# Kernel optimization log

Hardware: AMD Instinct MI355X
Metric: run time of the kernel (lower is better)

Reference implementation:

```python
import jax, jax.numpy as jnp
import numpy as np

EPS = 1e-5


def farthest_point_sample(points, npoint):
    # points: [B, N, 3]; returns idx [B, npoint] (int32)
    B, N, _ = points.shape
    # is_center=True: start from the point farthest from the centroid
    centroid = points.mean(axis=1, keepdims=True)            # [B,1,3]
    d0 = jnp.sum((points - centroid) ** 2, axis=-1)           # [B,N]
    farthest = jnp.argmax(d0, axis=-1)                        # [B]
    distance = jnp.full((B, N), 1e10, dtype=points.dtype)

    def step(carry, _):
        dist, far = carry
        cent = jnp.take_along_axis(points, far[:, None, None], axis=1)  # [B,1,3]
        d = jnp.sum((points - cent) ** 2, axis=-1)                       # [B,N]
        dist = jnp.minimum(dist, d)
        new_far = jnp.argmax(dist, axis=-1)
        return (dist, new_far), far

    (_, _), idx = jax.lax.scan(step, (distance, farthest), None, length=npoint)
    return idx.T  # [B, npoint]


def index_points(x, idx):
    # x: [B, N, C], idx: [B, S] -> [B, S, C]
    return jnp.take_along_axis(x, idx[:, :, None], axis=1)


def setup_inputs() -> dict:
    key = jax.random.key(0)
    k1, k2, k3, k4 = jax.random.split(key, 4)
    B, N, in_dim, out_dim = 8, 16384, 128, 256
    points = jax.random.normal(k1, (B, N, 3), dtype=jnp.float32)
    features = jax.random.normal(k2, (B, N, in_dim), dtype=jnp.float32)
    W = jax.random.normal(k3, (out_dim, in_dim), dtype=jnp.float32) * (1.0 / np.sqrt(in_dim))
    b = jax.random.normal(k4, (out_dim,), dtype=jnp.float32) * 0.01
    return {"points": points, "features": features, "W": W, "b": b, "num_points": 4096}


def reference(points, features, W, b, num_points):
    # conv1x1 on features.transpose(-1,-2): [B,in,N] -> [B,out,N]
    x = jnp.einsum('bnc,oc->bon', features, W) + b[None, :, None]  # [B,out,N]
    # InstanceNorm1d (affine=False): normalize over spatial dim N per (b, channel)
    mu = x.mean(axis=-1, keepdims=True)
    var = x.var(axis=-1, keepdims=True)
    x = (x - mu) * jax.lax.rsqrt(var + EPS)
    x = jax.nn.relu(x)
    feats = x.transpose(0, 2, 1)  # [B,N,out]

    idx = farthest_point_sample(points, num_points)  # [B, num_points]
    sampled_points = index_points(points, idx)
    sampled_features = index_points(feats, idx)
    return sampled_points, sampled_features
```

## Files before the change

kernel.cpp:

```cpp
#include <hip/hip_runtime.h>
#include <math.h>

#define B_      8
#define N_      16384
#define CIN_    128
#define COUT_   256
#define NS_     4096
#define FPS_T   1024
#define PPT     16

#define RPT16(X) X(0) X(1) X(2) X(3) X(4) X(5) X(6) X(7) \
                 X(8) X(9) X(10) X(11) X(12) X(13) X(14) X(15)

static __device__ __forceinline__ float sqdist_xla(float px, float py, float pz,
                                                   float cx, float cy, float cz) {
  float dx = __fsub_rn(px, cx);
  float dy = __fsub_rn(py, cy);
  float dz = __fsub_rn(pz, cz);
  return __fmaf_rn(dz, dz, __fmaf_rn(dy, dy, __fmul_rn(dx, dx)));
}

__global__ __launch_bounds__(1024, 4) void k1_fps_gram(
    const float* __restrict__ points, const float* __restrict__ features,
    float* __restrict__ outP, int* __restrict__ idxw,
    float* __restrict__ Gpart, float* __restrict__ Spart)
{
  const int tid = threadIdx.x;
  if (blockIdx.x < B_) {
    const int b = blockIdx.x;
    const float* __restrict__ P = points + (size_t)b * N_ * 3;
    const int base = tid * PPT;
    const int lane = tid & 63;
    const int wid  = tid >> 6;

    #define DECLP(i) float px##i, py##i, pz##i, dd##i;
    RPT16(DECLP)
    #define LOADP(i) px##i = P[3*(base+(i))+0]; \
                     py##i = P[3*(base+(i))+1]; \
                     pz##i = P[3*(base+(i))+2];
    RPT16(LOADP)

    __shared__ unsigned svv[16];
    __shared__ int      sii[16];
    __shared__ float    cC[3];
    __shared__ float    cent[3];

    if (tid < 3) {
      const int c = tid;
      float acc = P[c];
      for (int n = 1; n < N_; ++n) acc = __fadd_rn(acc, P[3*n + c]);
      cent[c] = __fmul_rn(acc, 6.103515625e-05f);
    }
    __syncthreads();
    const float cx0 = cent[0], cy0 = cent[1], cz0 = cent[2];

    auto select_far = [&](float lmv, int lkv, int s) {
      unsigned long long pk =
          ((unsigned long long)__float_as_uint(lmv) << 32) | (unsigned)(~(base + lkv));
      #pragma unroll
      for (int off = 32; off > 0; off >>= 1) {
        unsigned long long op = __shfl_xor(pk, off);
        pk = (op > pk) ? op : pk;
      }
      if (lane == 0) { svv[wid] = (unsigned)(pk >> 32); sii[wid] = (int)(~(unsigned)pk); }
      __syncthreads();
      if (wid == 0) {
        unsigned long long p2 = 0ULL;
        if (lane < 16)
          p2 = ((unsigned long long)svv[lane] << 32) | (unsigned)(~sii[lane]);
        #pragma unroll
        for (int off = 8; off > 0; off >>= 1) {
          unsigned long long op = __shfl_xor(p2, off);
          p2 = (op > p2) ? op : p2;
        }
        if (lane == 0) {
          const int bi = (int)(~(unsigned)p2);
          const float* cp = P + 3 * (size_t)bi;
          const float x = cp[0], y = cp[1], z = cp[2];
          cC[0] = x; cC[1] = y; cC[2] = z;
          const size_t ob = (size_t)b * NS_ + s;
          outP[ob*3+0] = x; outP[ob*3+1] = y; outP[ob*3+2] = z;
          idxw[b*NS_ + s] = bi;
        }
      }
      __syncthreads();
    };

    {
      float lm = -1.0f; int lk = 0;
      #define SCAN0(i) { float d = sqdist_xla(px##i, py##i, pz##i, cx0, cy0, cz0); \
                         dd##i = d; bool bt = (d > lm); \
                         lk = bt ? (i) : lk; lm = bt ? d : lm; }
      RPT16(SCAN0)
      select_far(lm, lk, 0);
    }
    #define INITD(i) dd##i = 1e10f;
    RPT16(INITD)

    for (int s = 1; s < NS_; ++s) {
      const float ccx = cC[0], ccy = cC[1], ccz = cC[2];
      float lm = -1.0f; int lk = 0;
      #define SCANU(i) { float d = sqdist_xla(px##i, py##i, pz##i, ccx, ccy, ccz); \
                         float nd = fminf(dd##i, d); dd##i = nd; \
                         bool bt = (nd > lm); \
                         lk = bt ? (i) : lk; lm = bt ? nd : lm; }
      RPT16(SCANU)
      select_far(lm, lk, s);
    }
  } else {
    const int gb = (int)blockIdx.x - B_;
    const int b  = gb >> 3;
    const int ch = gb & 7;
    __shared__ float Lf[32][128];
    float acc[4][4];
    #pragma unroll
    for (int i = 0; i < 4; ++i)
      #pragma unroll
      for (int j = 0; j < 4; ++j) acc[i][j] = 0.f;
    float sacc = 0.f;
    const int ti = tid >> 5;
    const int tj = tid & 31;
    const float* fb = features + ((size_t)b * N_ + (size_t)ch * 2048) * CIN_;
    for (int t32 = 0; t32 < 64; ++t32) {
      const float4 v0 = *(const float4*)(fb + ((size_t)t32 * 32 + ti) * CIN_ + tj * 4);
      __syncthreads();
      *(float4*)&Lf[ti][tj*4] = v0;
      __syncthreads();
      #pragma unroll 4
      for (int r = 0; r < 32; ++r) {
        const float4 a4 = *(const float4*)&Lf[r][ti*4];
        const float4 b4 = *(const float4*)&Lf[r][tj*4];
        const float av[4] = {a4.x, a4.y, a4.z, a4.w};
        const float bw[4] = {b4.x, b4.y, b4.z, b4.w};
        #pragma unroll
        for (int i = 0; i < 4; ++i)
          #pragma unroll
          for (int j = 0; j < 4; ++j) acc[i][j] = fmaf(av[i], bw[j], acc[i][j]);
      }
      if (tid < 128) {
        #pragma unroll 8
        for (int r = 0; r < 32; ++r) sacc += Lf[r][tid];
      }
    }
    float* gp = Gpart + (size_t)gb * (CIN_*CIN_);
    #pragma unroll
    for (int i = 0; i < 4; ++i)
      #pragma unroll
      for (int j = 0; j < 4; ++j)
        gp[(ti*4+i)*CIN_ + tj*4 + j] = acc[i][j];
    if (tid < 128) Spart[gb*CIN_ + tid] = sacc;
  }
}

__global__ void k2a_reduce(const float* __restrict__ Gpart, const float* __restrict__ Spart,
                           float* __restrict__ Gred, float* __restrict__ Sred)
{
  const int b = blockIdx.x;
  for (int i = threadIdx.x; i < CIN_*CIN_; i += blockDim.x) {
    float s = 0.f;
    #pragma unroll
    for (int c = 0; c < 8; ++c) s += Gpart[((size_t)(b*8+c))*(CIN_*CIN_) + i];
    Gred[(size_t)b*(CIN_*CIN_) + i] = s;
  }
  if (threadIdx.x < CIN_) {
    float s = 0.f;
    #pragma unroll
    for (int c = 0; c < 8; ++c) s += Spart[(b*8+c)*CIN_ + threadIdx.x];
    Sred[b*CIN_ + threadIdx.x] = s;
  }
}

__global__ __launch_bounds__(128) void k2b_stats(
    const float* __restrict__ Gred, const float* __restrict__ Sred,
    const float* __restrict__ W, const float* __restrict__ bias,
    float* __restrict__ stats)
{
  const int b = blockIdx.x >> 8;
  const int o = blockIdx.x & 255;
  const int tid = threadIdx.x;
  __shared__ float sw[CIN_];
  __shared__ float r1[CIN_], r2[CIN_];
  sw[tid] = W[(size_t)o*CIN_ + tid];
  __syncthreads();
  const float* gr = Gred + (size_t)b*CIN_*CIN_ + (size_t)tid*CIN_;
  float g = 0.f;
  #pragma unroll 8
  for (int j = 0; j < CIN_; ++j) g = fmaf(gr[j], sw[j], g);
  r1[tid] = g * sw[tid];
  r2[tid] = sw[tid] * Sred[b*CIN_ + tid];
  __syncthreads();
  for (int stp = 64; stp > 0; stp >>= 1) {
    if (tid < stp) { r1[tid] += r1[tid+stp]; r2[tid] += r2[tid+stp]; }
    __syncthreads();
  }
  if (tid == 0) {
    const float wGw = r1[0], wS = r2[0], bo = bias[o];
    const float invN = 1.0f / (float)N_;
    const float mu  = wS*invN + bo;
    const float ex2 = (wGw + 2.0f*bo*wS)*invN + bo*bo;
    float var = ex2 - mu*mu;
    var = fmaxf(var, 0.0f);
    const float sc = 1.0f / sqrtf(var + 1e-5f);
    stats[((size_t)(b*COUT_ + o))*2 + 0] = wS*invN;
    stats[((size_t)(b*COUT_ + o))*2 + 1] = sc;
  }
}

__global__ __launch_bounds__(256) void k3_out(
    const float* __restrict__ features, const float* __restrict__ W,
    const int* __restrict__ idxw, const float* __restrict__ stats,
    float* __restrict__ outF)
{
  const int tid = threadIdx.x;
  const int b  = blockIdx.x >> 8;
  const int r  = blockIdx.x & 255;
  const int st = r >> 2, ot = r & 3;
  const int s0 = st * 64, o0 = ot * 64;

  __shared__ float Fs[64][129];
  __shared__ float Wt[64][129];
  __shared__ int   sIdx[64];
  __shared__ float sSub[64], sSc[64];

  if (tid < 64) sIdx[tid] = idxw[b*NS_ + s0 + tid];
  if (tid >= 64 && tid < 128) {
    const int oo = tid - 64;
    sSub[oo] = stats[((size_t)(b*COUT_ + o0 + oo))*2 + 0];
    sSc[oo]  = stats[((size_t)(b*COUT_ + o0 + oo))*2 + 1];
  }
  __syncthreads();
  {
    const int row = tid >> 2;
    const int q   = tid & 3;
    const float* fsrc = features + ((size_t)b*N_ + sIdx[row]) * CIN_;
    const float* wsrc = W + (size_t)(o0 + row) * CIN_;
    #pragma unroll
    for (int v = 0; v < 8; ++v) {
      const int c = q*4 + v*16;
      const float4 fv = *(const float4*)(fsrc + c);
      const float4 wv = *(const float4*)(wsrc + c);
      Fs[row][c+0]=fv.x; Fs[row][c+1]=fv.y; Fs[row][c+2]=fv.z; Fs[row][c+3]=fv.w;
      Wt[row][c+0]=wv.x; Wt[row][c+1]=wv.y; Wt[row][c+2]=wv.z; Wt[row][c+3]=wv.w;
    }
  }
  __syncthreads();

  const int ts = tid >> 4, to = tid & 15;
  float acc[4][4];
  #pragma unroll
  for (int i = 0; i < 4; ++i)
    #pragma unroll
    for (int j = 0; j < 4; ++j) acc[i][j] = 0.f;

  #pragma unroll 4
  for (int k = 0; k < CIN_; ++k) {
    const float a0 = Fs[ts*4+0][k], a1 = Fs[ts*4+1][k], a2 = Fs[ts*4+2][k], a3 = Fs[ts*4+3][k];
    const float w0 = Wt[to*4+0][k], w1 = Wt[to*4+1][k], w2 = Wt[to*4+2][k], w3 = Wt[to*4+3][k];
    acc[0][0]=fmaf(a0,w0,acc[0][0]); acc[0][1]=fmaf(a0,w1,acc[0][1]); acc[0][2]=fmaf(a0,w2,acc[0][2]); acc[0][3]=fmaf(a0,w3,acc[0][3]);
    acc[1][0]=fmaf(a1,w0,acc[1][0]); acc[1][1]=fmaf(a1,w1,acc[1][1]); acc[1][2]=fmaf(a1,w2,acc[1][2]); acc[1][3]=fmaf(a1,w3,acc[1][3]);
    acc[2][0]=fmaf(a2,w0,acc[2][0]); acc[2][1]=fmaf(a2,w1,acc[2][1]); acc[2][2]=fmaf(a2,w2,acc[2][2]); acc[2][3]=fmaf(a2,w3,acc[2][3]);
    acc[3][0]=fmaf(a3,w0,acc[3][0]); acc[3][1]=fmaf(a3,w1,acc[3][1]); acc[3][2]=fmaf(a3,w2,acc[3][2]); acc[3][3]=fmaf(a3,w3,acc[3][3]);
  }

  #pragma unroll
  for (int i = 0; i < 4; ++i) {
    float4 o4;
    o4.x = fmaxf((acc[i][0] - sSub[to*4+0]) * sSc[to*4+0], 0.f);
    o4.y = fmaxf((acc[i][1] - sSub[to*4+1]) * sSc[to*4+1], 0.f);
    o4.z = fmaxf((acc[i][2] - sSub[to*4+2]) * sSc[to*4+2], 0.f);
    o4.w = fmaxf((acc[i][3] - sSub[to*4+3]) * sSc[to*4+3], 0.f);
    *(float4*)&outF[((size_t)b*NS_ + s0 + ts*4 + i)*COUT_ + o0 + to*4] = o4;
  }
}

extern "C" void kernel_launch(void* const* d_in, const int* in_sizes, int n_in,
                              void* d_out, int out_size, void* d_ws, size_t ws_size,
                              hipStream_t stream) {
  (void)in_sizes; (void)n_in; (void)out_size; (void)ws_size;
  const float* points   = (const float*)d_in[0];
  const float* features = (const float*)d_in[1];
  const float* W        = (const float*)d_in[2];
  const float* bias     = (const float*)d_in[3];
  float* out  = (float*)d_out;
  float* outP = out;
  float* outF = out + (size_t)B_*NS_*3;

  char* ws = (char*)d_ws;
  int*   idxw  = (int*)  (ws + 0);
  float* Gpart = (float*)(ws + 131072);
  float* Spart = (float*)(ws + 131072 + 4194304);
  float* Gred  = (float*)(ws + 131072 + 4194304 + 32768);
  float* Sred  = (float*)(ws + 131072 + 4194304 + 32768 + 524288);
  float* stats = (float*)(ws + 131072 + 4194304 + 32768 + 524288 + 4096);

  k1_fps_gram<<<dim3(B_ + 64), dim3(FPS_T), 0, stream>>>(points, features, outP, idxw, Gpart, Spart);
  k2a_reduce <<<dim3(B_),      dim3(512),   0, stream>>>(Gpart, Spart, Gred, Sred);
  k2b_stats  <<<dim3(B_*COUT_),dim3(CIN_),  0, stream>>>(Gred, Sred, W, bias, stats);
  k3_out     <<<dim3(B_*256),  dim3(256),   0, stream>>>(features, W, idxw, stats, outF);
}
```

Baseline: 7.012 ms.

## Use one barrier per FPS step with redundant per-wave final reduction

The FPS loop now does a single __syncthreads per iteration. Every wave reads the 16 per-wave candidates from a double-buffered LDS slot and reduces them itself, instead of wave 0 reducing and broadcasting through a second barrier. Point x/y coordinates move into a shared LDS buffer while z stays in registers. Points are laid out strided (i*1024+tid) so LDS reads are coalesced, which lowers register pressure. The cost is one LDS read per point per step and each wave loading the centroid from global memory, and the gram blocks now share the large LDS allocation, which may limit occupancy.

```diff
diff --git a/kernel.cpp b/kernel.cpp
--- a/kernel.cpp
+++ b/kernel.cpp
@@ -9,6 +9,8 @@
 #define FPS_T   1024
 #define PPT     16
 
+typedef unsigned long long ull_t;
+
 #define RPT16(X) X(0) X(1) X(2) X(3) X(4) X(5) X(6) X(7) \
                  X(8) X(9) X(10) X(11) X(12) X(13) X(14) X(15)
 
@@ -25,25 +27,27 @@
     float* __restrict__ outP, int* __restrict__ idxw,
     float* __restrict__ Gpart, float* __restrict__ Spart)
 {
+  __shared__ __align__(16) char LDSB[131072 + 256 + 16];
   const int tid = threadIdx.x;
+
   if (blockIdx.x < B_) {
+    float* __restrict__ sXY = (float*)LDSB;
+    ull_t* __restrict__ cand = (ull_t*)(LDSB + 131072);
+    float* __restrict__ cent = (float*)(LDSB + 131072 + 256);
+
     const int b = blockIdx.x;
     const float* __restrict__ P = points + (size_t)b * N_ * 3;
-    const int base = tid * PPT;
     const int lane = tid & 63;
     const int wid  = tid >> 6;
 
-    #define DECLP(i) float px##i, py##i, pz##i, dd##i;
+    #define DECLP(i) float z##i, dd##i;
     RPT16(DECLP)
-    #define LOADP(i) px##i = P[3*(base+(i))+0]; \
-                     py##i = P[3*(base+(i))+1]; \
-                     pz##i = P[3*(base+(i))+2];
+    #define LOADP(i) { const int n = (i)*1024 + tid; \
+      const float x = P[3*n+0], y = P[3*n+1]; z##i = P[3*n+2]; \
+      *(float2*)&sXY[2*n] = make_float2(x, y); }
     RPT16(LOADP)
-
-    __shared__ unsigned svv[16];
-    __shared__ int      sii[16];
-    __shared__ float    cC[3];
-    __shared__ float    cent[3];
+    #define PINZ(i) asm volatile("" : "+v"(z##i));
+    RPT16(PINZ)
 
     if (tid < 3) {
       const int c = tid;
@@ -54,64 +58,68 @@
     __syncthreads();
     const float cx0 = cent[0], cy0 = cent[1], cz0 = cent[2];
 
-    auto select_far = [&](float lmv, int lkv, int s) {
-      unsigned long long pk =
-          ((unsigned long long)__float_as_uint(lmv) << 32) | (unsigned)(~(base + lkv));
+    int far; float ccx, ccy, ccz;
+    auto select_far = [&](float lmv, int giv, int par) {
+      ull_t pk = ((ull_t)__float_as_uint(lmv) << 32) | (unsigned)(~giv);
       #pragma unroll
       for (int off = 32; off > 0; off >>= 1) {
-        unsigned long long op = __shfl_xor(pk, off);
+        ull_t op = __shfl_xor(pk, off);
         pk = (op > pk) ? op : pk;
       }
-      if (lane == 0) { svv[wid] = (unsigned)(pk >> 32); sii[wid] = (int)(~(unsigned)pk); }
+      if (lane == 0) cand[par*16 + wid] = pk;
       __syncthreads();
-      if (wid == 0) {
-        unsigned long long p2 = 0ULL;
-        if (lane < 16)
-          p2 = ((unsigned long long)svv[lane] << 32) | (unsigned)(~sii[lane]);
-        #pragma unroll
-        for (int off = 8; off > 0; off >>= 1) {
-          unsigned long long op = __shfl_xor(p2, off);
-          p2 = (op > p2) ? op : p2;
-        }
-        if (lane == 0) {
-          const int bi = (int)(~(unsigned)p2);
-          const float* cp = P + 3 * (size_t)bi;
-          const float x = cp[0], y = cp[1], z = cp[2];
-          cC[0] = x; cC[1] = y; cC[2] = z;
-          const size_t ob = (size_t)b * NS_ + s;
-          outP[ob*3+0] = x; outP[ob*3+1] = y; outP[ob*3+2] = z;
-          idxw[b*NS_ + s] = bi;
-        }
-      }
-      __syncthreads();
+      ull_t c2 = (lane < 16) ? cand[par*16 + lane] : 0ULL;
+      #pragma unroll
+      for (int off = 8; off > 0; off >>= 1) {
+        ull_t op = __shfl_xor(c2, off);
+        c2 = (op > c2) ? op : c2;
+      }
+      c2 = __shfl(c2, 0);
+      far = (int)(~(unsigned)c2);
+      const float* __restrict__ cp = P + 3 * (size_t)far;
+      ccx = cp[0]; ccy = cp[1]; ccz = cp[2];
     };
 
     {
-      float lm = -1.0f; int lk = 0;
-      #define SCAN0(i) { float d = sqdist_xla(px##i, py##i, pz##i, cx0, cy0, cz0); \
-                         dd##i = d; bool bt = (d > lm); \
-                         lk = bt ? (i) : lk; lm = bt ? d : lm; }
+      float lm; int lk = 0;
+      {
+        const float2 xy = *(const float2*)&sXY[2*tid];
+        lm = sqdist_xla(xy.x, xy.y, z0, cx0, cy0, cz0);
+      }
+      #define SCAN0(i) if ((i) > 0) { \
+        const float2 xy = *(const float2*)&sXY[2*((i)*1024 + tid)]; \
+        const float d = sqdist_xla(xy.x, xy.y, z##i, cx0, cy0, cz0); \
+        const bool bt = (d > lm); lk = bt ? (i) : lk; lm = bt ? d : lm; }
       RPT16(SCAN0)
-      select_far(lm, lk, 0);
+      select_far(lm, lk*1024 + tid, 0);
+      if (tid == 0) {
+        outP[(size_t)b*NS_*3 + 0] = ccx; outP[(size_t)b*NS_*3 + 1] = ccy;
+        outP[(size_t)b*NS_*3 + 2] = ccz; idxw[b*NS_] = far;
+      }
     }
     #define INITD(i) dd##i = 1e10f;
     RPT16(INITD)
 
     for (int s = 1; s < NS_; ++s) {
-      const float ccx = cC[0], ccy = cC[1], ccz = cC[2];
       float lm = -1.0f; int lk = 0;
-      #define SCANU(i) { float d = sqdist_xla(px##i, py##i, pz##i, ccx, ccy, ccz); \
-                         float nd = fminf(dd##i, d); dd##i = nd; \
-                         bool bt = (nd > lm); \
-                         lk = bt ? (i) : lk; lm = bt ? nd : lm; }
+      #define SCANU(i) { \
+        const float2 xy = *(const float2*)&sXY[2*((i)*1024 + tid)]; \
+        const float d  = sqdist_xla(xy.x, xy.y, z##i, ccx, ccy, ccz); \
+        const float nd = fminf(dd##i, d); dd##i = nd; \
+        const bool bt = (nd > lm); lk = bt ? (i) : lk; lm = bt ? nd : lm; }
       RPT16(SCANU)
-      select_far(lm, lk, s);
+      select_far(lm, lk*1024 + tid, s & 1);
+      if (tid == 0) {
+        const size_t ob = (size_t)b*NS_ + s;
+        outP[ob*3+0] = ccx; outP[ob*3+1] = ccy; outP[ob*3+2] = ccz;
+        idxw[ob] = far;
+      }
     }
   } else {
+    float* __restrict__ Lf = (float*)LDSB;
     const int gb = (int)blockIdx.x - B_;
     const int b  = gb >> 3;
     const int ch = gb & 7;
-    __shared__ float Lf[32][128];
     float acc[4][4];
     #pragma unroll
     for (int i = 0; i < 4; ++i)
@@ -124,12 +132,12 @@
     for (int t32 = 0; t32 < 64; ++t32) {
       const float4 v0 = *(const float4*)(fb + ((size_t)t32 * 32 + ti) * CIN_ + tj * 4);
       __syncthreads();
-      *(float4*)&Lf[ti][tj*4] = v0;
+      *(float4*)&Lf[ti*128 + tj*4] = v0;
       __syncthreads();
       #pragma unroll 4
       for (int r = 0; r < 32; ++r) {
-        const float4 a4 = *(const float4*)&Lf[r][ti*4];
-        const float4 b4 = *(const float4*)&Lf[r][tj*4];
+        const float4 a4 = *(const float4*)&Lf[r*128 + ti*4];
+        const float4 b4 = *(const float4*)&Lf[r*128 + tj*4];
         const float av[4] = {a4.x, a4.y, a4.z, a4.w};
         const float bw[4] = {b4.x, b4.y, b4.z, b4.w};
         #pragma unroll
@@ -139,7 +147,7 @@
       }
       if (tid < 128) {
         #pragma unroll 8
-        for (int r = 0; r < 32; ++r) sacc += Lf[r][tid];
+        for (int r = 0; r < 32; ++r) sacc += Lf[r*128 + tid];
       }
     }
     float* gp = Gpart + (size_t)gb * (CIN_*CIN_);
```

Result: slower. 7.895 ms (+12.6%).

## Cut FPS to 512 threads with single-barrier argmax and fuse Gram reduction

Applied to the files above, without the earlier changes.

The FPS blocks drop to 512 threads with 32 points each held in registers. The per-step argmax now packs value, index and wave id into one key and uses double-buffered shared slots, so each step needs one barrier instead of two and the winning coordinates come from registers rather than a global reload. The Gram-matrix side now runs one block per batch over all N rows with 4x8 register tiles and writes the reduced result directly, which removes the separate reduce kernel and the partial-sum buffers. The trade-offs are far fewer Gram blocks (8 instead of 64), so that work is less parallel, and higher register pressure in the FPS loop.

```diff
diff --git a/kernel.cpp b/kernel.cpp
--- a/kernel.cpp
+++ b/kernel.cpp
@@ -6,11 +6,14 @@
 #define CIN_    128
 #define COUT_   256
 #define NS_     4096
-#define FPS_T   1024
-#define PPT     16
-
-#define RPT16(X) X(0) X(1) X(2) X(3) X(4) X(5) X(6) X(7) \
-                 X(8) X(9) X(10) X(11) X(12) X(13) X(14) X(15)
+#define PPT     32
+
+typedef unsigned long long u64;
+
+#define RPT32(X) X(0) X(1) X(2) X(3) X(4) X(5) X(6) X(7) \
+                 X(8) X(9) X(10) X(11) X(12) X(13) X(14) X(15) \
+                 X(16) X(17) X(18) X(19) X(20) X(21) X(22) X(23) \
+                 X(24) X(25) X(26) X(27) X(28) X(29) X(30) X(31)
 
 static __device__ __forceinline__ float sqdist_xla(float px, float py, float pz,
                                                    float cx, float cy, float cz) {
@@ -20,12 +23,19 @@
   return __fmaf_rn(dz, dz, __fmaf_rn(dy, dy, __fmul_rn(dx, dx)));
 }
 
-__global__ __launch_bounds__(1024, 4) void k1_fps_gram(
+__global__ void
+__attribute__((amdgpu_flat_work_group_size(512, 512), amdgpu_waves_per_eu(2, 2)))
+k1_fps_gram(
     const float* __restrict__ points, const float* __restrict__ features,
     float* __restrict__ outP, int* __restrict__ idxw,
-    float* __restrict__ Gpart, float* __restrict__ Spart)
+    float* __restrict__ Gred, float* __restrict__ Sred)
 {
+  __shared__ u64   slotKey[2][8];
+  __shared__ float slotC[2][8][4];
+  __shared__ float cent[3];
+  __shared__ __align__(16) float Lf[32][128];
   const int tid = threadIdx.x;
+
   if (blockIdx.x < B_) {
     const int b = blockIdx.x;
     const float* __restrict__ P = points + (size_t)b * N_ * 3;
@@ -33,17 +43,14 @@
     const int lane = tid & 63;
     const int wid  = tid >> 6;
 
-    #define DECLP(i) float px##i, py##i, pz##i, dd##i;
-    RPT16(DECLP)
-    #define LOADP(i) px##i = P[3*(base+(i))+0]; \
-                     py##i = P[3*(base+(i))+1]; \
-                     pz##i = P[3*(base+(i))+2];
-    RPT16(LOADP)
-
-    __shared__ unsigned svv[16];
-    __shared__ int      sii[16];
-    __shared__ float    cC[3];
-    __shared__ float    cent[3];
+    #define DECLP(i) float x##i, y##i, z##i, dd##i;
+    RPT32(DECLP)
+    #define LOADP(i) x##i = P[3*(base+(i))+0]; \
+                     y##i = P[3*(base+(i))+1]; \
+                     z##i = P[3*(base+(i))+2];
+    RPT32(LOADP)
+    #define PINP(i) asm volatile("" : "+v"(x##i), "+v"(y##i), "+v"(z##i));
+    RPT32(PINP)
 
     if (tid < 3) {
       const int c = tid;
@@ -52,121 +59,107 @@
       cent[c] = __fmul_rn(acc, 6.103515625e-05f);
     }
     __syncthreads();
-    const float cx0 = cent[0], cy0 = cent[1], cz0 = cent[2];
-
-    auto select_far = [&](float lmv, int lkv, int s) {
-      unsigned long long pk =
-          ((unsigned long long)__float_as_uint(lmv) << 32) | (unsigned)(~(base + lkv));
-      #pragma unroll
-      for (int off = 32; off > 0; off >>= 1) {
-        unsigned long long op = __shfl_xor(pk, off);
-        pk = (op > pk) ? op : pk;
-      }
-      if (lane == 0) { svv[wid] = (unsigned)(pk >> 32); sii[wid] = (int)(~(unsigned)pk); }
-      __syncthreads();
-      if (wid == 0) {
-        unsigned long long p2 = 0ULL;
-        if (lane < 16)
-          p2 = ((unsigned long long)svv[lane] << 32) | (unsigned)(~sii[lane]);
-        #pragma unroll
-        for (int off = 8; off > 0; off >>= 1) {
-          unsigned long long op = __shfl_xor(p2, off);
-          p2 = (op > p2) ? op : p2;
-        }
-        if (lane == 0) {
-          const int bi = (int)(~(unsigned)p2);
-          const float* cp = P + 3 * (size_t)bi;
-          const float x = cp[0], y = cp[1], z = cp[2];
-          cC[0] = x; cC[1] = y; cC[2] = z;
-          const size_t ob = (size_t)b * NS_ + s;
-          outP[ob*3+0] = x; outP[ob*3+1] = y; outP[ob*3+2] = z;
-          idxw[b*NS_ + s] = bi;
-        }
-      }
-      __syncthreads();
-    };
+
+    float ccx, ccy, ccz;
+
+    #define PICKI(i) { const bool e = (lk == (i)); \
+      sx = e ? x##i : sx; sy = e ? y##i : sy; sz = e ? z##i : sz; }
+
+    #define SELECT_FAR(pp, ss) do { \
+      const int gid = base + lk; \
+      const u64 my = ((u64)__float_as_uint(lm) << 32) \
+                   | ((u64)((unsigned)(~gid) & 0x3FFFu) << 4) | (unsigned)wid; \
+      u64 wk = my; \
+      _Pragma("unroll") \
+      for (int off = 32; off > 0; off >>= 1) { \
+        const u64 o = __shfl_xor(wk, off); wk = (o > wk) ? o : wk; } \
+      if (my == wk) { \
+        float sx = x0, sy = y0, sz = z0; \
+        RPT32(PICKI) \
+        slotKey[pp][wid] = wk; \
+        slotC[pp][wid][0] = sx; slotC[pp][wid][1] = sy; slotC[pp][wid][2] = sz; \
+      } \
+      __syncthreads(); \
+      u64 bk2 = slotKey[pp][lane & 7]; \
+      _Pragma("unroll") \
+      for (int off = 4; off > 0; off >>= 1) { \
+        const u64 o = __shfl_xor(bk2, off); bk2 = (o > bk2) ? o : bk2; } \
+      const int wsl = (int)(bk2 & 7); \
+      ccx = slotC[pp][wsl][0]; ccy = slotC[pp][wsl][1]; ccz = slotC[pp][wsl][2]; \
+      if (tid == 0) { \
+        const size_t ob = (size_t)b * NS_ + (ss); \
+        outP[ob*3+0] = ccx; outP[ob*3+1] = ccy; outP[ob*3+2] = ccz; \
+        idxw[ob] = (int)((~(bk2 >> 4)) & 0x3FFFULL); \
+      } \
+    } while (0)
 
     {
+      const float cx0 = cent[0], cy0 = cent[1], cz0 = cent[2];
+      float lm; int lk = 0;
+      lm = sqdist_xla(x0, y0, z0, cx0, cy0, cz0); dd0 = lm;
+      #define SCAN0(i) if ((i) > 0) { \
+        const float d = sqdist_xla(x##i, y##i, z##i, cx0, cy0, cz0); \
+        dd##i = d; const bool bt = (d > lm); \
+        lk = bt ? (i) : lk; lm = bt ? d : lm; }
+      RPT32(SCAN0)
+      SELECT_FAR(0, 0);
+    }
+    #define INITD(i) dd##i = 1e10f;
+    RPT32(INITD)
+
+    for (int s = 1; s < NS_; ++s) {
       float lm = -1.0f; int lk = 0;
-      #define SCAN0(i) { float d = sqdist_xla(px##i, py##i, pz##i, cx0, cy0, cz0); \
-                         dd##i = d; bool bt = (d > lm); \
-                         lk = bt ? (i) : lk; lm = bt ? d : lm; }
-      RPT16(SCAN0)
-      select_far(lm, lk, 0);
-    }
-    #define INITD(i) dd##i = 1e10f;
-    RPT16(INITD)
-
-    for (int s = 1; s < NS_; ++s) {
-      const float ccx = cC[0], ccy = cC[1], ccz = cC[2];
-      float lm = -1.0f; int lk = 0;
-      #define SCANU(i) { float d = sqdist_xla(px##i, py##i, pz##i, ccx, ccy, ccz); \
-                         float nd = fminf(dd##i, d); dd##i = nd; \
-                         bool bt = (nd > lm); \
-                         lk = bt ? (i) : lk; lm = bt ? nd : lm; }
-      RPT16(SCANU)
-      select_far(lm, lk, s);
+      #define SCANU(i) { \
+        const float d  = sqdist_xla(x##i, y##i, z##i, ccx, ccy, ccz); \
+        const float nd = fminf(dd##i, d); dd##i = nd; \
+        const bool bt = (nd > lm); \
+        lk = bt ? (i) : lk; lm = bt ? nd : lm; }
+      RPT32(SCANU)
+      SELECT_FAR(s & 1, s);
     }
   } else {
-    const int gb = (int)blockIdx.x - B_;
-    const int b  = gb >> 3;
-    const int ch = gb & 7;
-    __shared__ float Lf[32][128];
-    float acc[4][4];
+    const int b = (int)blockIdx.x - B_;
+    float acc[4][8];
     #pragma unroll
     for (int i = 0; i < 4; ++i)
       #pragma unroll
-      for (int j = 0; j < 4; ++j) acc[i][j] = 0.f;
+      for (int j = 0; j < 8; ++j) acc[i][j] = 0.f;
     float sacc = 0.f;
-    const int ti = tid >> 5;
-    const int tj = tid & 31;
-    const float* fb = features + ((size_t)b * N_ + (size_t)ch * 2048) * CIN_;
-    for (int t32 = 0; t32 < 64; ++t32) {
-      const float4 v0 = *(const float4*)(fb + ((size_t)t32 * 32 + ti) * CIN_ + tj * 4);
+    const int ti = tid >> 4;
+    const int tj = tid & 15;
+    const float* fb = features + (size_t)b * N_ * CIN_;
+    for (int t32 = 0; t32 < N_/32; ++t32) {
+      const float* src = fb + ((size_t)t32 * 32 + ti) * CIN_ + tj * 8;
+      const float4 v0 = *(const float4*)(src);
+      const float4 v1 = *(const float4*)(src + 4);
       __syncthreads();
-      *(float4*)&Lf[ti][tj*4] = v0;
+      *(float4*)&Lf[ti][tj*8]     = v0;
+      *(float4*)&Lf[ti][tj*8 + 4] = v1;
       __syncthreads();
       #pragma unroll 4
       for (int r = 0; r < 32; ++r) {
-        const float4 a4 = *(const float4*)&Lf[r][ti*4];
-        const float4 b4 = *(const float4*)&Lf[r][tj*4];
+        const float4 a4  = *(const float4*)&Lf[r][ti*4];
+        const float4 b40 = *(const float4*)&Lf[r][tj*8];
+        const float4 b41 = *(const float4*)&Lf[r][tj*8+4];
         const float av[4] = {a4.x, a4.y, a4.z, a4.w};
-        const float bw[4] = {b4.x, b4.y, b4.z, b4.w};
+        const float bw[8] = {b40.x, b40.y, b40.z, b40.w, b41.x, b41.y, b41.z, b41.w};
         #pragma unroll
         for (int i = 0; i < 4; ++i)
           #pragma unroll
-          for (int j = 0; j < 4; ++j) acc[i][j] = fmaf(av[i], bw[j], acc[i][j]);
+          for (int j = 0; j < 8; ++j) acc[i][j] = fmaf(av[i], bw[j], acc[i][j]);
       }
       if (tid < 128) {
         #pragma unroll 8
         for (int r = 0; r < 32; ++r) sacc += Lf[r][tid];
       }
     }
-    float* gp = Gpart + (size_t)gb * (CIN_*CIN_);
+    float* gp = Gred + (size_t)b * (CIN_*CIN_);
     #pragma unroll
     for (int i = 0; i < 4; ++i)
       #pragma unroll
-      for (int j = 0; j < 4; ++j)
-        gp[(ti*4+i)*CIN_ + tj*4 + j] = acc[i][j];
-    if (tid < 128) Spart[gb*CIN_ + tid] = sacc;
-  }
-}
-
-__global__ void k2a_reduce(const float* __restrict__ Gpart, const float* __restrict__ Spart,
-                           float* __restrict__ Gred, float* __restrict__ Sred)
-{
-  const int b = blockIdx.x;
-  for (int i = threadIdx.x; i < CIN_*CIN_; i += blockDim.x) {
-    float s = 0.f;
-    #pragma unroll
-    for (int c = 0; c < 8; ++c) s += Gpart[((size_t)(b*8+c))*(CIN_*CIN_) + i];
-    Gred[(size_t)b*(CIN_*CIN_) + i] = s;
-  }
-  if (threadIdx.x < CIN_) {
-    float s = 0.f;
-    #pragma unroll
-    for (int c = 0; c < 8; ++c) s += Spart[(b*8+c)*CIN_ + threadIdx.x];
-    Sred[b*CIN_ + threadIdx.x] = s;
+      for (int j = 0; j < 8; ++j)
+        gp[(ti*4+i)*CIN_ + tj*8 + j] = acc[i][j];
+    if (tid < 128) Sred[b*CIN_ + tid] = sacc;
   }
 }
 
@@ -287,14 +280,11 @@
 
   char* ws = (char*)d_ws;
   int*   idxw  = (int*)  (ws + 0);
-  float* Gpart = (float*)(ws + 131072);
-  float* Spart = (float*)(ws + 131072 + 4194304);
-  float* Gred  = (float*)(ws + 131072 + 4194304 + 32768);
-  float* Sred  = (float*)(ws + 131072 + 4194304 + 32768 + 524288);
-  float* stats = (float*)(ws + 131072 + 4194304 + 32768 + 524288 + 4096);
-
-  k1_fps_gram<<<dim3(B_ + 64), dim3(FPS_T), 0, stream>>>(points, features, outP, idxw, Gpart, Spart);
-  k2a_reduce <<<dim3(B_),      dim3(512),   0, stream>>>(Gpart, Spart, Gred, Sred);
-  k2b_stats  <<<dim3(B_*COUT_),dim3(CIN_),  0, stream>>>(Gred, Sred, W, bias, stats);
-  k3_out     <<<dim3(B_*256),  dim3(256),   0, stream>>>(features, W, idxw, stats, outF);
-}
+  float* Gred  = (float*)(ws + 131072);
+  float* Sred  = (float*)(ws + 655360);
+  float* stats = (float*)(ws + 659456);
+
+  k1_fps_gram<<<dim3(B_ + B_),  dim3(512),  0, stream>>>(points, features, outP, idxw, Gred, Sred);
+  k2b_stats  <<<dim3(B_*COUT_), dim3(CIN_), 0, stream>>>(Gred, Sred, W, bias, stats);
+  k3_out     <<<dim3(B_*256),   dim3(256),  0, stream>>>(features, W, idxw, stats, outF);
+}
```

Result: slower. 9.231 ms (+31.6%).
